# Optimization experiments

Hardware: AMD Instinct MI355X
Metric: run time of the kernel (lower is better)

The kernel has to match this reference:

```python
import jax, jax.numpy as jnp
import numpy as np

N = 6144      # total nodes
G = 32        # graphs
NPG = 192     # nodes per graph (N = G*NPG)
FIN = 32      # num_node_features
FE = 8        # num_edge_features
H = 64        # layers = [64, 64]
HM = 128      # layers_MLP = [128]
C = 2         # num_classes
K = 8         # opts.knn
E = 49152     # given edges
EPS = 1e-5


def _bn(x, g, b):
    # BatchNorm1d in train mode: biased batch stats
    m = x.mean(0)
    v = x.var(0)
    return (x - m) * jax.lax.rsqrt(v + EPS) * g + b


def setup_inputs() -> dict:
    key = jax.random.key(0)
    ks = jax.random.split(key, 24)

    def w(k, shape):
        return (jax.random.normal(k, shape, jnp.float32)
                * (1.0 / np.sqrt(shape[0])).astype(np.float32))

    x = jax.random.normal(ks[0], (N, FIN), jnp.float32)
    edge_index = jax.random.randint(ks[1], (2, E), 0, N)
    edge_attr = jax.random.normal(ks[2], (E, FE), jnp.float32)
    batch = jnp.arange(N, dtype=jnp.int64 if jax.config.jax_enable_x64 else jnp.int32) // NPG
    return dict(
        x=x, edge_index=edge_index, edge_attr=edge_attr, batch=batch,
        # EdgeFeatsConv layer 1: mlp(Linear(2*FIN+FE,H), ReLU, Linear(H,H)) + root weight
        ef_w1=w(ks[3], (2 * FIN + FE, H)), ef_b1=jnp.zeros((H,), jnp.float32),
        ef_w2=w(ks[4], (H, H)), ef_b2=jnp.zeros((H,), jnp.float32),
        ef_wroot=w(ks[5], (FIN, H)),
        bn1_g=jnp.ones((H,), jnp.float32), bn1_b=jnp.zeros((H,), jnp.float32),
        # EdgeConv layer 2: mlp(Linear(2*H,H), ReLU, Linear(H,H)), aggr=max
        ec_w1=w(ks[6], (2 * H, H)), ec_b1=jnp.zeros((H,), jnp.float32),
        ec_w2=w(ks[7], (H, H)), ec_b2=jnp.zeros((H,), jnp.float32),
        bn2_g=jnp.ones((H,), jnp.float32), bn2_b=jnp.zeros((H,), jnp.float32),
        # model2: Linear(H,HM), BN, ReLU, Linear(HM,C)
        m2_w1=w(ks[8], (H, HM)), m2_b1=jnp.zeros((HM,), jnp.float32),
        m2_bng=jnp.ones((HM,), jnp.float32), m2_bnb=jnp.zeros((HM,), jnp.float32),
        m2_w2=w(ks[9], (HM, C)), m2_b2=jnp.zeros((C,), jnp.float32),
    )


def reference(x, edge_index, edge_attr, batch,
              ef_w1, ef_b1, ef_w2, ef_b2, ef_wroot, bn1_g, bn1_b,
              ec_w1, ec_b1, ec_w2, ec_b2, bn2_g, bn2_b,
              m2_w1, m2_b1, m2_bng, m2_bnb, m2_w2, m2_b2):
    src, dst = edge_index[0], edge_index[1]

    # ---- layer 1: EdgeFeatsConv (edge-conditioned message MLP + root weight, aggr=sum)
    m = jnp.concatenate([x[dst], x[src], edge_attr], axis=1) @ ef_w1 + ef_b1
    m = jax.nn.relu(m) @ ef_w2 + ef_b2
    x1 = jax.ops.segment_sum(m, dst, num_segments=N) + x @ ef_wroot
    x1 = _bn(x1, bn1_g, bn1_b)

    # ---- layer 2: dynamic KNN graph (loop=False) + to_undirected, then EdgeConv (aggr=max)
    sq = jnp.sum(x1 * x1, axis=1)
    d2 = sq[:, None] + sq[None, :] - 2.0 * (x1 @ x1.T)       # [N, N]
    d2 = d2.at[jnp.arange(N), jnp.arange(N)].set(jnp.inf)    # no self loops
    _, nbr = jax.lax.top_k(-d2, K)                           # [N, K] nearest neighbors
    dst0 = jnp.repeat(jnp.arange(N), K)
    src0 = nbr.reshape(-1)
    s = jnp.concatenate([src0, dst0])                        # undirected (dups OK: max aggr)
    d = jnp.concatenate([dst0, src0])

    h = jnp.concatenate([x1[d], x1[s] - x1[d]], axis=1) @ ec_w1 + ec_b1
    h = jax.nn.relu(h) @ ec_w2 + ec_b2
    x2 = jax.ops.segment_max(h, d, num_segments=N)
    x2 = _bn(x2, bn2_g, bn2_b)

    # ---- per-graph all-pairs |g_i - g_z| (row order: for z, for i)
    g = x2.reshape(G, NPG, H)
    diff = jnp.abs(g[:, None, :, :] - g[:, :, None, :]).reshape(-1, H)  # [G*NPG*NPG, H]

    # ---- model2 MLP + log_softmax
    h2 = jax.nn.relu(_bn(diff @ m2_w1 + m2_b1, m2_bng, m2_bnb))
    out = h2 @ m2_w2 + m2_b2
    return jax.nn.log_softmax(out, axis=1)
```

## Files before the change

### kernel.cpp

```cpp
#include <hip/hip_runtime.h>

#define NN 6144
#define GG 32
#define NPGc 192
#define FINc 32
#define FEc 8
#define Hc 64
#define HMc 128
#define Kc 8
#define Ec 49152
#define NKc (NN*Kc)
#define RTOTc (GG*NPGc*NPGc)

typedef float f32x4 __attribute__((ext_vector_type(4)));
typedef short bf16x8 __attribute__((ext_vector_type(8)));
typedef unsigned long long u64;

__device__ __forceinline__ unsigned short f2bf(float f){
  unsigned u = __float_as_uint(f);
  unsigned r = u + 0x7fffu + ((u>>16)&1u);
  return (unsigned short)(r>>16);
}
__device__ __forceinline__ unsigned fenc(float f){
  unsigned u = __float_as_uint(f);
  return (u & 0x80000000u) ? ~u : (u | 0x80000000u);
}
__device__ __forceinline__ float fdec(unsigned e){
  unsigned u = (e & 0x80000000u) ? (e & 0x7fffffffu) : ~e;
  return __uint_as_float(u);
}
__device__ __forceinline__ void bub8(u64* t8, u64 k){
#pragma unroll
  for (int q=0;q<8;q++){ u64 cur=t8[q]; u64 lo=(k<cur)?k:cur; u64 hi=(k<cur)?cur:k; t8[q]=lo; k=hi; }
}

__global__ void k_init(float* dbins, float* stats){
  int idx = blockIdx.x*256 + threadIdx.x;
  if (idx < 64*256) dbins[idx] = 0.f;
  if (idx < 768) stats[idx] = 0.f;
}

__global__ __launch_bounds__(256) void k_root(const float* __restrict__ x, const float* __restrict__ wr, float* __restrict__ x1a){
  __shared__ float Ws[FINc*Hc];
  __shared__ float xr[4][FINc];
  int t = threadIdx.x;
  for (int q=t;q<FINc*Hc;q+=256) Ws[q] = wr[q];
  int rg = t>>6, j = t&63;
  int r = blockIdx.x*4 + rg;
  if (j < FINc) xr[rg][j] = x[r*FINc + j];
  __syncthreads();
  float a0=0.f, a1=0.f;
#pragma unroll
  for (int k=0;k<FINc;k+=2){
    a0 = fmaf(xr[rg][k],   Ws[k*Hc+j],     a0);
    a1 = fmaf(xr[rg][k+1], Ws[(k+1)*Hc+j], a1);
  }
  x1a[r*Hc + j] = a0 + a1;
}

__global__ __launch_bounds__(256) void k_eac(const float* __restrict__ ea, const float* __restrict__ w1, float* __restrict__ EAc){
  __shared__ float Wc[FEc*Hc];
  int t = threadIdx.x;
  for (int q=t; q<FEc*Hc; q+=256) Wc[q] = w1[64*Hc + q];
  __syncthreads();
  int idx = blockIdx.x*256 + t;
  int e = idx >> 4, c4 = (idx & 15)*4;
  float av[8];
#pragma unroll
  for (int q=0;q<8;q++) av[q] = ea[e*FEc + q];
  float4 o = {0.f,0.f,0.f,0.f};
#pragma unroll
  for (int q=0;q<8;q++){
    o.x = fmaf(av[q], Wc[q*Hc + c4+0], o.x);
    o.y = fmaf(av[q], Wc[q*Hc + c4+1], o.y);
    o.z = fmaf(av[q], Wc[q*Hc + c4+2], o.z);
    o.w = fmaf(av[q], Wc[q*Hc + c4+3], o.w);
  }
  *(float4*)(EAc + (size_t)e*Hc + c4) = o;
}

__global__ __launch_bounds__(256) void k_p12(const float* __restrict__ x, const float* __restrict__ w1, const float* __restrict__ b1,
                                             float* __restrict__ P1, float* __restrict__ P2){
  __shared__ float xs[16][32];
  int t = threadIdx.x;
  int j = t & 63, w = t >> 6;
  float wa[32], wb[32];
#pragma unroll
  for (int k=0;k<32;k++){
    wa[k] = w1[k*Hc + j];
    wb[k] = w1[(32+k)*Hc + j];
  }
  float b1j = b1[j];
  int nb = blockIdx.x * 16;
  for (int q=t; q<16*32; q+=256) xs[q>>5][q&31] = x[(size_t)(nb + (q>>5))*FINc + (q&31)];
  __syncthreads();
#pragma unroll
  for (int it=0; it<4; it++){
    int nl = it*4 + w;
    float a = b1j, b = 0.f;
#pragma unroll
    for (int k=0;k<32;k++){
      float xv = xs[nl][k];
      a = fmaf(xv, wa[k], a);
      b = fmaf(xv, wb[k], b);
    }
    int n = nb + nl;
    P1[(size_t)n*Hc + j] = a;
    P2[(size_t)n*Hc + j] = b;
  }
}

__global__ void k_zero_cnt(unsigned* rcnt){
  int idx = blockIdx.x*256 + threadIdx.x;
  if (idx < NN) rcnt[idx] = 0u;
}
__global__ void k_cnt_dst(const int* __restrict__ ei, unsigned* __restrict__ rcnt){
  int e = blockIdx.x*256 + threadIdx.x;
  atomicAdd(&rcnt[ei[Ec + e]], 1u);
}
__global__ __launch_bounds__(256) void k_scan(const unsigned* __restrict__ rcnt, unsigned* __restrict__ rptr, unsigned* __restrict__ rcur){
  __shared__ unsigned ps[256];
  int t = threadIdx.x;
  unsigned loc[24];
  unsigned s = 0;
#pragma unroll
  for (int q=0;q<24;q++){ loc[q] = s; s += rcnt[t*24+q]; }
  ps[t] = s;
  __syncthreads();
  for (int off=1; off<256; off<<=1){
    unsigned v = (t>=off)? ps[t-off] : 0u;
    __syncthreads();
    ps[t] += v;
    __syncthreads();
  }
  unsigned base = (t==0)? 0u : ps[t-1];
#pragma unroll
  for (int q=0;q<24;q++){ unsigned v = base + loc[q]; rptr[t*24+q]=v; rcur[t*24+q]=v; }
  if (t==255) rptr[NN] = ps[255];
}
__global__ void k_fill_dst(const int* __restrict__ ei, unsigned* __restrict__ rcur, unsigned* __restrict__ rlist){
  int e = blockIdx.x*256 + threadIdx.x;
  unsigned pos = atomicAdd(&rcur[ei[Ec + e]], 1u);
  rlist[pos] = (unsigned)e;
}
__global__ void k_rev_cnt(const unsigned* __restrict__ nbr, unsigned* __restrict__ rcnt){
  int e = blockIdx.x*256 + threadIdx.x;
  atomicAdd(&rcnt[nbr[e]], 1u);
}
__global__ void k_rev_fill(const unsigned* __restrict__ nbr, unsigned* __restrict__ rcur, unsigned* __restrict__ rlist){
  int e = blockIdx.x*256 + threadIdx.x;
  unsigned pos = atomicAdd(&rcur[nbr[e]], 1u);
  rlist[pos] = (unsigned)(e >> 3);
}

__global__ __launch_bounds__(128) void k_node1(const float* __restrict__ P1, const float* __restrict__ P2, const float* __restrict__ EAc,
        const int* __restrict__ ei, const unsigned* __restrict__ rptr, const unsigned* __restrict__ rlist,
        const float* __restrict__ w2, const float* __restrict__ b2, float* __restrict__ x1a){
  __shared__ __align__(16) float accs[16][68];
  __shared__ __align__(16) float W2T[64][68];
  __shared__ unsigned rp_s[17];
  int t = threadIdx.x;
  int d0 = blockIdx.x * 16;
  for (int q=t; q<64*64; q+=128) W2T[q&63][q>>6] = w2[q];
  if (t < 17) rp_s[t] = rptr[d0 + t];
  __syncthreads();
  int slot = t>>3, cg = t&7, c0 = cg*8;
  int n = d0 + slot;
  float4 p1a = *(const float4*)(P1 + (size_t)n*Hc + c0);
  float4 p1b = *(const float4*)(P1 + (size_t)n*Hc + c0 + 4);
  float acc[8];
#pragma unroll
  for (int q=0;q<8;q++) acc[q] = 0.f;
  unsigned beg = rp_s[slot], end = rp_s[slot+1];
  for (unsigned pos=beg; pos<end; pos++){
    unsigned e = rlist[pos];
    int s = ei[e];
    float4 qa = *(const float4*)(P2 + (size_t)s*Hc + c0);
    float4 qb = *(const float4*)(P2 + (size_t)s*Hc + c0 + 4);
    float4 fa = *(const float4*)(EAc + (size_t)e*Hc + c0);
    float4 fb = *(const float4*)(EAc + (size_t)e*Hc + c0 + 4);
    acc[0] += fmaxf(p1a.x + qa.x + fa.x, 0.f);
    acc[1] += fmaxf(p1a.y + qa.y + fa.y, 0.f);
    acc[2] += fmaxf(p1a.z + qa.z + fa.z, 0.f);
    acc[3] += fmaxf(p1a.w + qa.w + fa.w, 0.f);
    acc[4] += fmaxf(p1b.x + qb.x + fb.x, 0.f);
    acc[5] += fmaxf(p1b.y + qb.y + fb.y, 0.f);
    acc[6] += fmaxf(p1b.z + qb.z + fb.z, 0.f);
    acc[7] += fmaxf(p1b.w + qb.w + fb.w, 0.f);
  }
  *(float4*)&accs[slot][c0]   = make_float4(acc[0],acc[1],acc[2],acc[3]);
  *(float4*)&accs[slot][c0+4] = make_float4(acc[4],acc[5],acc[6],acc[7]);
  __syncthreads();
  float out[8];
#pragma unroll
  for (int q=0;q<8;q++) out[q] = 0.f;
  for (int k4=0;k4<16;k4++){
    float4 hv = *(const float4*)&accs[slot][k4*4];
#pragma unroll
    for (int cc=0;cc<8;cc++){
      float4 wv = *(const float4*)&W2T[c0+cc][k4*4];
      out[cc] = fmaf(hv.x,wv.x, fmaf(hv.y,wv.y, fmaf(hv.z,wv.z, fmaf(hv.w,wv.w, out[cc]))));
    }
  }
  float deg = (float)(end - beg);
  float* px = x1a + (size_t)n*Hc + c0;
#pragma unroll
  for (int cc=0;cc<8;cc++) px[cc] += out[cc] + deg*b2[c0+cc];
}

__global__ __launch_bounds__(256) void k_bn_stats(const float* __restrict__ src, float* __restrict__ gsum, float* __restrict__ gss){
  int t = threadIdx.x;
  int c = t & 63;
  int r0 = blockIdx.x*64 + (t>>6);
  float s=0.f, ss=0.f;
  for (int it=0; it<16; it++){
    int r = r0 + it*4;
    float v = src[r*Hc + c];
    s += v; ss += v*v;
  }
  __shared__ float S[64], SS[64];
  if (t < 64){ S[t]=0.f; SS[t]=0.f; }
  __syncthreads();
  atomicAdd(&S[c], s); atomicAdd(&SS[c], ss);
  __syncthreads();
  if (t < 64){ atomicAdd(&gsum[t], S[t]); atomicAdd(&gss[t], SS[t]); }
}

__global__ void k_bn_fin(const float* gsum, const float* gss, const float* gam, const float* bet, float* sc, float* sh){
  int c = threadIdx.x;
  float mean = gsum[c] / (float)NN;
  float var  = gss[c] / (float)NN - mean*mean;
  float rs = rsqrtf(var + 1e-5f);
  float s = rs * gam[c];
  sc[c] = s; sh[c] = bet[c] - mean*s;
}

__global__ __launch_bounds__(256) void k_apply_bn1_sq(const float* __restrict__ x1a, const float* __restrict__ sc, const float* __restrict__ sh,
                               float* __restrict__ x1bn, float* __restrict__ sqv){
  int t = threadIdx.x;
  int c = t & 63;
  int r = blockIdx.x*4 + (t>>6);
  float v = x1a[r*Hc + c]*sc[c] + sh[c];
  x1bn[r*Hc + c] = v;
  float s = v*v;
#pragma unroll
  for (int off=1; off<64; off<<=1) s += __shfl_xor(s, off, 64);
  if (c == 0) sqv[r] = s;
}

__global__ __launch_bounds__(128,2) void k_knn(const float* __restrict__ x1bn, const float* __restrict__ sqv, u64* __restrict__ parts, int CH){
  __shared__ __align__(16) float XJ[64][68];
  __shared__ float sqj[64];
  int t = threadIdx.x;
  int i1 = blockIdx.x*256 + t;
  int i2 = i1 + 128;
  float4 xa[16], xb[16];
#pragma unroll
  for (int q=0;q<16;q++){
    xa[q] = *(const float4*)(x1bn + (size_t)i1*Hc + q*4);
    xb[q] = *(const float4*)(x1bn + (size_t)i2*Hc + q*4);
  }
  float sqi1 = sqv[i1], sqi2 = sqv[i2];
  u64 t8a[8], t8b[8];
#pragma unroll
  for (int q=0;q<8;q++){ t8a[q] = ~0ull; t8b[q] = ~0ull; }
  float thra = __uint_as_float(0x7f800000u);
  float thrb = thra;
  int cpc = NN / CH;
  int nsub = cpc >> 6;
  int jbase0 = blockIdx.y * cpc;
  for (int sub=0; sub<nsub; sub++){
    int jb = jbase0 + sub*64;
    __syncthreads();
    {
      int c = t>>1, hh = t&1;
      const float4* srcp = (const float4*)(x1bn + (size_t)(jb + c)*Hc + hh*32);
#pragma unroll
      for (int q=0;q<8;q++) *(float4*)&XJ[c][hh*32 + q*4] = srcp[q];
      if (t < 64) sqj[t] = sqv[jb + t];
    }
    __syncthreads();
    for (int j=0;j<64;j++){
      float sqjc = sqj[j];
      float a0=0.f,a1=0.f,a2=0.f,a3=0.f,b0=0.f,b1=0.f,b2=0.f,b3=0.f;
#pragma unroll
      for (int q4=0;q4<4;q4++){
        float4 xj0 = *(const float4*)&XJ[j][q4*16];
        float4 xj1 = *(const float4*)&XJ[j][q4*16+4];
        float4 xj2 = *(const float4*)&XJ[j][q4*16+8];
        float4 xj3 = *(const float4*)&XJ[j][q4*16+12];
        float4 A0 = xa[q4*4+0], A1 = xa[q4*4+1], A2v = xa[q4*4+2], A3 = xa[q4*4+3];
        float4 B0 = xb[q4*4+0], B1 = xb[q4*4+1], B2v = xb[q4*4+2], B3 = xb[q4*4+3];
        a0=fmaf(A0.x,xj0.x,a0); a1=fmaf(A0.y,xj0.y,a1); a2=fmaf(A0.z,xj0.z,a2); a3=fmaf(A0.w,xj0.w,a3);
        b0=fmaf(B0.x,xj0.x,b0); b1=fmaf(B0.y,xj0.y,b1); b2=fmaf(B0.z,xj0.z,b2); b3=fmaf(B0.w,xj0.w,b3);
        a0=fmaf(A1.x,xj1.x,a0); a1=fmaf(A1.y,xj1.y,a1); a2=fmaf(A1.z,xj1.z,a2); a3=fmaf(A1.w,xj1.w,a3);
        b0=fmaf(B1.x,xj1.x,b0); b1=fmaf(B1.y,xj1.y,b1); b2=fmaf(B1.z,xj1.z,b2); b3=fmaf(B1.w,xj1.w,b3);
        a0=fmaf(A2v.x,xj2.x,a0); a1=fmaf(A2v.y,xj2.y,a1); a2=fmaf(A2v.z,xj2.z,a2); a3=fmaf(A2v.w,xj2.w,a3);
        b0=fmaf(B2v.x,xj2.x,b0); b1=fmaf(B2v.y,xj2.y,b1); b2=fmaf(B2v.z,xj2.z,b2); b3=fmaf(B2v.w,xj2.w,b3);
        a0=fmaf(A3.x,xj3.x,a0); a1=fmaf(A3.y,xj3.y,a1); a2=fmaf(A3.z,xj3.z,a2); a3=fmaf(A3.w,xj3.w,a3);
        b0=fmaf(B3.x,xj3.x,b0); b1=fmaf(B3.y,xj3.y,b1); b2=fmaf(B3.z,xj3.z,b2); b3=fmaf(B3.w,xj3.w,b3);
      }
      float dot1 = (a0+a1)+(a2+a3);
      float dot2 = (b0+b1)+(b2+b3);
      int jj = jb + j;
      float d2a = (sqi1 + sqjc) - 2.f*dot1;
      float d2b = (sqi2 + sqjc) - 2.f*dot2;
      bool ia = !(d2a > thra) && (jj != i1);
      bool ib = !(d2b > thrb) && (jj != i2);
      if (__builtin_expect(ia | ib, 0)){
        if (ia){
          u64 ka = (((u64)fenc(d2a))<<32) | (unsigned)jj;
          bub8(t8a, ka);
          thra = fdec((unsigned)(t8a[7]>>32));
        }
        if (ib){
          u64 kb = (((u64)fenc(d2b))<<32) | (unsigned)jj;
          bub8(t8b, kb);
          thrb = fdec((unsigned)(t8b[7]>>32));
        }
      }
    }
  }
  u64* pa = parts + ((size_t)blockIdx.y*NN + i1)*8;
  u64* pb = parts + ((size_t)blockIdx.y*NN + i2)*8;
#pragma unroll
  for (int q=0;q<8;q++){ pa[q] = t8a[q]; pb[q] = t8b[q]; }
}

__global__ __launch_bounds__(256) void k_knn_merge(const u64* __restrict__ parts, int CH, unsigned* __restrict__ nbr){
  int r = blockIdx.x*256 + threadIdx.x;
  u64 t8[8];
#pragma unroll
  for (int q=0;q<8;q++) t8[q] = ~0ull;
  for (int ch=0; ch<CH; ch++){
    const u64* p = parts + ((size_t)ch*NN + r)*8;
    u64 k[8];
#pragma unroll
    for (int q=0;q<8;q++) k[q] = p[q];
#pragma unroll
    for (int q=0;q<8;q++){
      if (k[q] >= t8[7]) break;
      bub8(t8, k[q]);
    }
  }
#pragma unroll
  for (int s=0;s<8;s++) nbr[r*Kc + s] = (unsigned)(t8[s] & 0xffffffffu);
}

__global__ __launch_bounds__(256) void k_pq(const float* __restrict__ x1bn, const float* __restrict__ w1, const float* __restrict__ b1,
                                            float* __restrict__ A2, float* __restrict__ Qm){
  __shared__ float xs[16][64];
  int t = threadIdx.x;
  int j = t & 63, w = t >> 6;
  float wa[64], wb[64];
#pragma unroll
  for (int k=0;k<64;k++){
    float wt  = w1[k*64 + j];
    float wbv = w1[(64+k)*64 + j];
    wa[k] = wt - wbv; wb[k] = wbv;
  }
  float b1j = b1[j];
  int nb = blockIdx.x * 16;
  for (int q=t; q<16*64; q+=256) xs[q>>6][q&63] = x1bn[(size_t)(nb + (q>>6))*64 + (q&63)];
  __syncthreads();
#pragma unroll
  for (int it=0; it<4; it++){
    int nl = it*4 + w;
    float a = b1j, qq = 0.f;
#pragma unroll
    for (int k=0;k<64;k++){
      float xv = xs[nl][k];
      a  = fmaf(xv, wa[k], a);
      qq = fmaf(xv, wb[k], qq);
    }
    int n = nb + nl;
    A2[(size_t)n*64 + j] = a;
    Qm[(size_t)n*64 + j] = qq;
  }
}

__global__ __launch_bounds__(128) void k_edge2max(const float* __restrict__ A2, const float* __restrict__ Qm,
        const unsigned* __restrict__ nbr, const unsigned* __restrict__ rptr, const unsigned* __restrict__ rlist,
        const float* __restrict__ w2, const float* __restrict__ b2, float* __restrict__ x2f){
  __shared__ __align__(16) float W2T[64][68];
  __shared__ __align__(16) float hidT[64][132];
  __shared__ unsigned x2s[17][64];
  __shared__ unsigned rp_s[17];
  __shared__ int wslot[128];
  int t = threadIdx.x;
  int d0 = blockIdx.x * 16;
  for (int q=t; q<64*64; q+=128) W2T[q&63][q>>6] = w2[q];
  for (int q=t; q<17*64; q+=128) ((unsigned*)x2s)[q] = 0x007FFFFFu;
  if (t < 17) rp_s[t] = rptr[d0 + t];
  __syncthreads();
  unsigned rp0 = rp_s[0];
  int total_rev = (int)(rp_s[16] - rp0);
  int eg = t & 15, cg = t >> 4;
  int r0 = eg*8, c0 = cg*8;
  float b2v[8];
#pragma unroll
  for (int cc=0;cc<8;cc++) b2v[cc] = b2[c0+cc];
  int ntile = 1 + ((total_rev + 127) >> 7);
  for (int tile=0; tile<ntile; tile++){
    int d, s, active;
    if (tile == 0){
      d = d0 + (t>>3); s = (int)nbr[(size_t)d*8 + (t&7)]; active = 1; wslot[t] = t>>3;
    } else {
      int idx = (tile-1)*128 + t;
      active = idx < total_rev;
      if (active){
        unsigned pos = rp0 + (unsigned)idx;
        int sl = 0;
#pragma unroll
        for (int m=1; m<16; m++) sl += (pos >= rp_s[m]) ? 1 : 0;
        s = (int)rlist[pos];
        d = d0 + sl;
        wslot[t] = sl;
      } else { d = d0; s = 0; wslot[t] = 16; }
    }
    if (active){
      const float* pa = A2 + (size_t)d*64;
      const float* pq = Qm + (size_t)s*64;
#pragma unroll
      for (int c4=0; c4<16; c4++){
        float4 va = *(const float4*)(pa + c4*4);
        float4 vq = *(const float4*)(pq + c4*4);
        hidT[c4*4+0][t] = fmaxf(va.x+vq.x, 0.f);
        hidT[c4*4+1][t] = fmaxf(va.y+vq.y, 0.f);
        hidT[c4*4+2][t] = fmaxf(va.z+vq.z, 0.f);
        hidT[c4*4+3][t] = fmaxf(va.w+vq.w, 0.f);
      }
    } else {
#pragma unroll
      for (int c4=0; c4<16; c4++){
        hidT[c4*4+0][t] = 0.f; hidT[c4*4+1][t] = 0.f;
        hidT[c4*4+2][t] = 0.f; hidT[c4*4+3][t] = 0.f;
      }
    }
    __syncthreads();
    float acc[8][8];
#pragma unroll
    for (int i=0;i<8;i++)
#pragma unroll
      for (int cc=0;cc<8;cc++) acc[i][cc] = 0.f;
    for (int k=0;k<64;k+=4){
      float4 wv[8];
#pragma unroll
      for (int cc=0;cc<8;cc++) wv[cc] = *(const float4*)&W2T[c0+cc][k];
#pragma unroll
      for (int kk=0;kk<4;kk++){
        float4 h0 = *(const float4*)&hidT[k+kk][r0];
        float4 h1 = *(const float4*)&hidT[k+kk][r0+4];
        float hh[8] = {h0.x,h0.y,h0.z,h0.w,h1.x,h1.y,h1.z,h1.w};
#pragma unroll
        for (int i=0;i<8;i++)
#pragma unroll
          for (int cc=0;cc<8;cc++)
            acc[i][cc] = fmaf(hh[i], ((const float*)&wv[cc])[kk], acc[i][cc]);
      }
    }
    int cur = wslot[r0];
    float mx[8];
#pragma unroll
    for (int cc=0;cc<8;cc++) mx[cc] = acc[0][cc];
    for (int i=1;i<8;i++){
      int sl = wslot[r0+i];
      if (sl != cur){
#pragma unroll
        for (int cc=0;cc<8;cc++) atomicMax(&x2s[cur][c0+cc], fenc(mx[cc] + b2v[cc]));
        cur = sl;
#pragma unroll
        for (int cc=0;cc<8;cc++) mx[cc] = acc[i][cc];
      } else {
#pragma unroll
        for (int cc=0;cc<8;cc++) mx[cc] = fmaxf(mx[cc], acc[i][cc]);
      }
    }
#pragma unroll
    for (int cc=0;cc<8;cc++) atomicMax(&x2s[cur][c0+cc], fenc(mx[cc] + b2v[cc]));
    __syncthreads();
  }
#pragma unroll
  for (int q=0;q<8;q++){
    int idx = t + q*128;
    int sl = idx >> 6, c = idx & 63;
    x2f[(size_t)(d0+sl)*64 + c] = fdec(x2s[sl][c]);
  }
}

__global__ __launch_bounds__(256) void k_apply_bn2f(const float* __restrict__ x2f, const float* __restrict__ sc, const float* __restrict__ sh, float* __restrict__ x2bn){
  int idx = blockIdx.x*256 + threadIdx.x;
  int c = idx & 63;
  x2bn[idx] = x2f[idx]*sc[c] + sh[c];
}

__global__ __launch_bounds__(256,2) void k_d_stats(const float* __restrict__ x2bn, const float* __restrict__ w1, float* __restrict__ dbins){
  __shared__ __align__(16) char sm[24576 + 16384 + 1024];
  unsigned char* A = (unsigned char*)sm;
  unsigned char* W = (unsigned char*)sm + 24576;
  float* Ssum = (float*)(sm + 40960);
  int t = threadIdx.x;
  int gid = blockIdx.x; int g = gid / NPGc; int z = gid - g*NPGc;
  const float* xg = x2bn + (size_t)g*NPGc*Hc;
  const float* xz = xg + z*Hc;
  Ssum[t] = 0.f;
#pragma unroll
  for (int q=0;q<8;q++){
    int task = t + 256*q; int c = task & 127; int c4 = task >> 7;
    ushort4 p;
    p.x = f2bf(w1[(4*c4+0)*HMc + c]);
    p.y = f2bf(w1[(4*c4+1)*HMc + c]);
    p.z = f2bf(w1[(4*c4+2)*HMc + c]);
    p.w = f2bf(w1[(4*c4+3)*HMc + c]);
    *(ushort4*)(W + c*128 + ((c4*8) ^ ((c&7)<<4))) = p;
  }
#pragma unroll
  for (int q=0;q<12;q++){
    int task = t + 256*q; int i = task >> 4; int c = task & 15;
    float4 a = *(const float4*)(xg + i*Hc + c*4);
    float4 b = *(const float4*)(xz + c*4);
    ushort4 p;
    p.x = f2bf(fabsf(a.x-b.x)); p.y = f2bf(fabsf(a.y-b.y));
    p.z = f2bf(fabsf(a.z-b.z)); p.w = f2bf(fabsf(a.w-b.w));
    *(ushort4*)(A + i*128 + ((c*8) ^ ((i&7)<<4))) = p;
  }
  __syncthreads();
  int w = t>>6, l = t&63, lr = l&15, lg = l>>4;
  int sw = (lr&7)<<4;
  f32x4 zero = {0.f,0.f,0.f,0.f};
  f32x4 acc[3][8];
#pragma unroll
  for (int r=0;r<3;r++)
#pragma unroll
    for (int c=0;c<8;c++) acc[r][c] = zero;
#pragma unroll
  for (int kk=0;kk<2;kk++){
    bf16x8 af[3], bfr[8];
#pragma unroll
    for (int r=0;r<3;r++){
      int row = (w*3+r)*16 + lr;
      af[r] = *(const bf16x8*)(A + row*128 + ((lg*16 + 64*kk) ^ sw));
    }
#pragma unroll
    for (int c=0;c<8;c++){
      int col = c*16 + lr;
      bfr[c] = *(const bf16x8*)(W + col*128 + ((lg*16 + 64*kk) ^ sw));
    }
#pragma unroll
    for (int r=0;r<3;r++)
#pragma unroll
      for (int c=0;c<8;c++)
        acc[r][c] = __builtin_amdgcn_mfma_f32_16x16x32_bf16(af[r], bfr[c], acc[r][c], 0,0,0);
  }
#pragma unroll
  for (int c=0;c<8;c++){
    int col = c*16 + lr;
    float s=0.f, ss=0.f;
#pragma unroll
    for (int r=0;r<3;r++)
#pragma unroll
      for (int q=0;q<4;q++){ float v = acc[r][c][q]; s += v; ss = fmaf(v,v,ss); }
    s  += __shfl_xor(s, 16, 64);  ss += __shfl_xor(ss, 16, 64);
    s  += __shfl_xor(s, 32, 64);  ss += __shfl_xor(ss, 32, 64);
    if (lg == 0){
      atomicAdd(&Ssum[col], s);
      atomicAdd(&Ssum[128+col], ss);
    }
  }
  __syncthreads();
  if (t < 128){
    int bin = gid & 63;
    atomicAdd(&dbins[bin*256 + t], Ssum[t]);
    atomicAdd(&dbins[bin*256 + 128 + t], Ssum[128+t]);
  }
}

__global__ void k_d_fin(const float* __restrict__ dbins, const float* gam, const float* bet, float* dsc, float* dsh){
  int c = threadIdx.x;
  float s=0.f, ss=0.f;
#pragma unroll 8
  for (int b=0;b<64;b++){ s += dbins[b*256 + c]; ss += dbins[b*256 + 128 + c]; }
  float mean = s / (float)RTOTc;
  float var  = ss / (float)RTOTc - mean*mean;
  float rs = rsqrtf(var + 1e-5f);
  float k = rs * gam[c];
  dsc[c] = k; dsh[c] = bet[c] - mean*k;
}

__global__ __launch_bounds__(256,2) void k_d_main(const float* __restrict__ x2bn, const float* __restrict__ w1,
                         const float* __restrict__ w2, const float* __restrict__ b2g,
                         const float* __restrict__ dsc, const float* __restrict__ dsh, float* __restrict__ out){
  __shared__ __align__(16) char sm[49152 + 4096 + 1024];
  unsigned char* A   = (unsigned char*)sm;
  unsigned char* W   = (unsigned char*)sm + 24576;
  unsigned char* W2T = (unsigned char*)sm + 49152;
  float* sS = (float*)(sm + 53248);
  int t = threadIdx.x;
  int gid = blockIdx.x; int g = gid / NPGc; int z = gid - g*NPGc;
  const float* xg = x2bn + (size_t)g*NPGc*Hc;
  const float* xz = xg + z*Hc;
  if (t < 128){ sS[t] = dsc[t]; sS[128+t] = dsh[t]; }
  {
    int c = t>>4, kc = t&15;
    ushort4 p0 = make_ushort4(0,0,0,0), p1 = make_ushort4(0,0,0,0);
    if (c < 2){
      p0.x = f2bf(w2[(kc*8+0)*2 + c]); p0.y = f2bf(w2[(kc*8+1)*2 + c]);
      p0.z = f2bf(w2[(kc*8+2)*2 + c]); p0.w = f2bf(w2[(kc*8+3)*2 + c]);
      p1.x = f2bf(w2[(kc*8+4)*2 + c]); p1.y = f2bf(w2[(kc*8+5)*2 + c]);
      p1.z = f2bf(w2[(kc*8+6)*2 + c]); p1.w = f2bf(w2[(kc*8+7)*2 + c]);
    }
    int byte = c*256 + ((kc*16) ^ ((c&7)<<4));
    *(ushort4*)(W2T + byte) = p0;
    *(ushort4*)(W2T + byte + 8) = p1;
  }
#pragma unroll
  for (int q=0;q<8;q++){
    int task = t + 256*q; int c = task & 127; int c4 = task >> 7;
    ushort4 p;
    p.x = f2bf(w1[(4*c4+0)*HMc + c]);
    p.y = f2bf(w1[(4*c4+1)*HMc + c]);
    p.z = f2bf(w1[(4*c4+2)*HMc + c]);
    p.w = f2bf(w1[(4*c4+3)*HMc + c]);
    *(ushort4*)(W + c*128 + ((c4*8) ^ ((c&7)<<4))) = p;
  }
#pragma unroll
  for (int q=0;q<12;q++){
    int task = t + 256*q; int i = task >> 4; int c = task & 15;
    float4 a = *(const float4*)(xg + i*Hc + c*4);
    float4 b = *(const float4*)(xz + c*4);
    ushort4 p;
    p.x = f2bf(fabsf(a.x-b.x)); p.y = f2bf(fabsf(a.y-b.y));
    p.z = f2bf(fabsf(a.z-b.z)); p.w = f2bf(fabsf(a.w-b.w));
    *(ushort4*)(A + i*128 + ((c*8) ^ ((i&7)<<4))) = p;
  }
  __syncthreads();
  int w = t>>6, l = t&63, lr = l&15, lg = l>>4;
  int sw = (lr&7)<<4;
  f32x4 zero = {0.f,0.f,0.f,0.f};
  f32x4 acc[3][8];
#pragma unroll
  for (int r=0;r<3;r++)
#pragma unroll
    for (int c=0;c<8;c++) acc[r][c] = zero;
#pragma unroll
  for (int kk=0;kk<2;kk++){
    bf16x8 af[3], bfr[8];
#pragma unroll
    for (int r=0;r<3;r++){
      int row = (w*3+r)*16 + lr;
      af[r] = *(const bf16x8*)(A + row*128 + ((lg*16 + 64*kk) ^ sw));
    }
#pragma unroll
    for (int c=0;c<8;c++){
      int col = c*16 + lr;
      bfr[c] = *(const bf16x8*)(W + col*128 + ((lg*16 + 64*kk) ^ sw));
    }
#pragma unroll
    for (int r=0;r<3;r++)
#pragma unroll
      for (int c=0;c<8;c++)
        acc[r][c] = __builtin_amdgcn_mfma_f32_16x16x32_bf16(af[r], bfr[c], acc[r][c], 0,0,0);
  }
  __syncthreads();
#pragma unroll
  for (int r=0;r<3;r++){
#pragma unroll
    for (int c=0;c<8;c++){
      int col = c*16 + lr;
      float scl = sS[col], shf = sS[128+col];
#pragma unroll
      for (int q=0;q<4;q++){
        int row = (w*3+r)*16 + lg*4 + q;
        float v = fmaxf(acc[r][c][q]*scl + shf, 0.f);
        *(unsigned short*)(A + row*256 + ((col*2) ^ ((row&7)<<4))) = f2bf(v);
      }
    }
  }
  __syncthreads();
  f32x4 acc2[3];
#pragma unroll
  for (int r=0;r<3;r++) acc2[r] = zero;
#pragma unroll
  for (int kk=0;kk<4;kk++){
    bf16x8 bw = *(const bf16x8*)(W2T + lr*256 + ((lg*16 + 64*kk) ^ sw));
#pragma unroll
    for (int r=0;r<3;r++){
      int row = (w*3+r)*16 + lr;
      bf16x8 ah = *(const bf16x8*)(A + row*256 + ((lg*16 + 64*kk) ^ sw));
      acc2[r] = __builtin_amdgcn_mfma_f32_16x16x32_bf16(ah, bw, acc2[r], 0,0,0);
    }
  }
  float b2a = b2g[0], b2b = b2g[1];
  size_t obase = (size_t)gid * NPGc;
#pragma unroll
  for (int r=0;r<3;r++){
#pragma unroll
    for (int q=0;q<4;q++){
      float o = acc2[r][q];
      float oo = __shfl_xor(o, 1, 64);
      if (lr < 2){
        int row = (w*3+r)*16 + lg*4 + q;
        float self = o + ((lr==0) ? b2a : b2b);
        float oth  = oo + ((lr==0) ? b2b : b2a);
        float mx = fmaxf(self, oth);
        float lse = mx + logf(expf(self-mx) + expf(oth-mx));
        out[(obase + row)*2 + lr] = self - lse;
      }
    }
  }
}

extern "C" void kernel_launch(void* const* d_in, const int* in_sizes, int n_in,
                              void* d_out, int out_size, void* d_ws, size_t ws_size,
                              hipStream_t stream){
  const float* x    = (const float*)d_in[0];
  const int*   ei   = (const int*)d_in[1];
  const float* ea   = (const float*)d_in[2];
  const float* efw1 = (const float*)d_in[4];
  const float* efb1 = (const float*)d_in[5];
  const float* efw2 = (const float*)d_in[6];
  const float* efb2 = (const float*)d_in[7];
  const float* efwr = (const float*)d_in[8];
  const float* bn1g = (const float*)d_in[9];
  const float* bn1b = (const float*)d_in[10];
  const float* ecw1 = (const float*)d_in[11];
  const float* ecb1 = (const float*)d_in[12];
  const float* ecw2 = (const float*)d_in[13];
  const float* ecb2 = (const float*)d_in[14];
  const float* bn2g = (const float*)d_in[15];
  const float* bn2b = (const float*)d_in[16];
  const float* m2w1 = (const float*)d_in[17];
  const float* m2bng = (const float*)d_in[19];
  const float* m2bnb = (const float*)d_in[20];
  const float* m2w2  = (const float*)d_in[21];
  const float* m2b2  = (const float*)d_in[22];

  char* ws = (char*)d_ws;
  float*    x1a   = (float*)(ws + 0);
  float*    x1bn  = (float*)(ws + 1572864);
  float*    x2bn  = (float*)(ws + 3145728);
  float*    x2f   = (float*)(ws + 4718592);
  float*    sqv   = (float*)(ws + 6291456);
  unsigned* nbr   = (unsigned*)(ws + 6316032);
  float*    stats = (float*)(ws + 6512640);
  float*    dbins = (float*)(ws + 6515712);
  u64*      parts = (u64*)(ws + 6581248);
  float*    A2    = (float*)(ws + 0);
  float*    Qm    = (float*)(ws + 3145728);
  float*    P1    = (float*)(ws + 3145728);
  float*    P2    = (float*)(ws + 4718592);
  unsigned* rcnt  = (unsigned*)(ws + 6581248);
  unsigned* rptr  = rcnt + 6400;
  unsigned* rcur  = rptr + 6400;
  unsigned* rlist = rcur + 6400;
  float*    EAc   = (float*)(ws + 6581248 + 4194304);
  float *g1sum = stats,     *g1ss = stats+64,  *sc1 = stats+128, *sh1 = stats+192;
  float *g2sum = stats+256, *g2ss = stats+320, *sc2 = stats+384, *sh2 = stats+448;
  float *dsc = stats+512, *dsh = stats+640;
  float* outp = (float*)d_out;

  int CH = 96;
  if (ws_size < 6581248ull + (size_t)NN*96*64) CH = 48;
  if (ws_size < 6581248ull + (size_t)NN*48*64) CH = 24;

  k_init<<<64,256,0,stream>>>(dbins, stats);
  k_root<<<1536,256,0,stream>>>(x, efwr, x1a);
  k_eac<<<3072,256,0,stream>>>(ea, efw1, EAc);
  k_zero_cnt<<<24,256,0,stream>>>(rcnt);
  k_cnt_dst<<<192,256,0,stream>>>(ei, rcnt);
  k_scan<<<1,256,0,stream>>>(rcnt, rptr, rcur);
  k_fill_dst<<<192,256,0,stream>>>(ei, rcur, rlist);
  k_p12<<<384,256,0,stream>>>(x, efw1, efb1, P1, P2);
  k_node1<<<384,128,0,stream>>>(P1, P2, EAc, ei, rptr, rlist, efw2, efb2, x1a);
  k_bn_stats<<<96,256,0,stream>>>(x1a, g1sum, g1ss);
  k_bn_fin<<<1,64,0,stream>>>(g1sum, g1ss, bn1g, bn1b, sc1, sh1);
  k_apply_bn1_sq<<<1536,256,0,stream>>>(x1a, sc1, sh1, x1bn, sqv);
  dim3 kg(24, CH);
  k_knn<<<kg,128,0,stream>>>(x1bn, sqv, parts, CH);
  k_knn_merge<<<24,256,0,stream>>>(parts, CH, nbr);
  k_zero_cnt<<<24,256,0,stream>>>(rcnt);
  k_rev_cnt<<<192,256,0,stream>>>(nbr, rcnt);
  k_scan<<<1,256,0,stream>>>(rcnt, rptr, rcur);
  k_rev_fill<<<192,256,0,stream>>>(nbr, rcur, rlist);
  k_pq<<<384,256,0,stream>>>(x1bn, ecw1, ecb1, A2, Qm);
  k_edge2max<<<384,128,0,stream>>>(A2, Qm, nbr, rptr, rlist, ecw2, ecb2, x2f);
  k_bn_stats<<<96,256,0,stream>>>(x2f, g2sum, g2ss);
  k_bn_fin<<<1,64,0,stream>>>(g2sum, g2ss, bn2g, bn2b, sc2, sh2);
  k_apply_bn2f<<<1536,256,0,stream>>>(x2f, sc2, sh2, x2bn);
  k_d_stats<<<6144,256,0,stream>>>(x2bn, m2w1, dbins);
  k_d_fin<<<1,128,0,stream>>>(dbins, m2bng, m2bnb, dsc, dsh);
  k_d_main<<<6144,256,0,stream>>>(x2bn, m2w1, m2w2, m2b2, dsc, dsh, outp);
}
```

Before: 554.1 us.

## Precompute bf16 MLP weights, fuse BN finalize, split KNN merge into two stages

Adds a one-time kernel that converts and swizzles the model2 weights to bf16, so the 6144-block d_stats and d_main kernels just copy them into shared memory instead of converting per block. BN finalize kernels are removed and their math is folded into the apply kernels. The KNN partial merge is split into a parallel group merge plus a final 8-way merge, and the number of KNN column chunks is reduced to 48. This trades extra workspace and per-block redundant BN math for fewer launches and more merge parallelism.

```diff
diff --git a/kernel.cpp b/kernel.cpp
--- a/kernel.cpp
+++ b/kernel.cpp
@@ -38,6 +38,33 @@
   int idx = blockIdx.x*256 + threadIdx.x;
   if (idx < 64*256) dbins[idx] = 0.f;
   if (idx < 768) stats[idx] = 0.f;
+}
+
+__global__ void k_prep_w(const float* __restrict__ w1, const float* __restrict__ w2,
+                         unsigned short* __restrict__ Wpre, unsigned short* __restrict__ W2Tp){
+  int idx = blockIdx.x*256 + threadIdx.x;
+  if (idx < 2048){
+    int c = idx >> 4, c4 = idx & 15;
+    ushort4 p;
+    p.x = f2bf(w1[(4*c4+0)*HMc + c]);
+    p.y = f2bf(w1[(4*c4+1)*HMc + c]);
+    p.z = f2bf(w1[(4*c4+2)*HMc + c]);
+    p.w = f2bf(w1[(4*c4+3)*HMc + c]);
+    *(ushort4*)((char*)Wpre + c*128 + ((c4*8) ^ ((c&7)<<4))) = p;
+  } else if (idx < 2304){
+    int t2 = idx - 2048;
+    int c = t2>>4, kc = t2&15;
+    ushort4 p0 = make_ushort4(0,0,0,0), p1 = make_ushort4(0,0,0,0);
+    if (c < 2){
+      p0.x = f2bf(w2[(kc*8+0)*2 + c]); p0.y = f2bf(w2[(kc*8+1)*2 + c]);
+      p0.z = f2bf(w2[(kc*8+2)*2 + c]); p0.w = f2bf(w2[(kc*8+3)*2 + c]);
+      p1.x = f2bf(w2[(kc*8+4)*2 + c]); p1.y = f2bf(w2[(kc*8+5)*2 + c]);
+      p1.z = f2bf(w2[(kc*8+6)*2 + c]); p1.w = f2bf(w2[(kc*8+7)*2 + c]);
+    }
+    int byte = c*256 + ((kc*16) ^ ((c&7)<<4));
+    *(ushort4*)((char*)W2Tp + byte) = p0;
+    *(ushort4*)((char*)W2Tp + byte + 8) = p1;
+  }
 }
 
 __global__ __launch_bounds__(256) void k_root(const float* __restrict__ x, const float* __restrict__ wr, float* __restrict__ x1a){
@@ -226,21 +253,23 @@
   if (t < 64){ atomicAdd(&gsum[t], S[t]); atomicAdd(&gss[t], SS[t]); }
 }
 
-__global__ void k_bn_fin(const float* gsum, const float* gss, const float* gam, const float* bet, float* sc, float* sh){
-  int c = threadIdx.x;
-  float mean = gsum[c] / (float)NN;
-  float var  = gss[c] / (float)NN - mean*mean;
-  float rs = rsqrtf(var + 1e-5f);
-  float s = rs * gam[c];
-  sc[c] = s; sh[c] = bet[c] - mean*s;
-}
-
-__global__ __launch_bounds__(256) void k_apply_bn1_sq(const float* __restrict__ x1a, const float* __restrict__ sc, const float* __restrict__ sh,
+__global__ __launch_bounds__(256) void k_apply_bn1_sq(const float* __restrict__ x1a,
+                               const float* __restrict__ gsum, const float* __restrict__ gss,
+                               const float* __restrict__ gam, const float* __restrict__ bet,
                                float* __restrict__ x1bn, float* __restrict__ sqv){
-  int t = threadIdx.x;
+  __shared__ float scs[64], shs[64];
+  int t = threadIdx.x;
+  if (t < 64){
+    float mean = gsum[t] / (float)NN;
+    float var  = gss[t] / (float)NN - mean*mean;
+    float rs = rsqrtf(var + 1e-5f);
+    float s = rs * gam[t];
+    scs[t] = s; shs[t] = bet[t] - mean*s;
+  }
+  __syncthreads();
   int c = t & 63;
   int r = blockIdx.x*4 + (t>>6);
-  float v = x1a[r*Hc + c]*sc[c] + sh[c];
+  float v = x1a[r*Hc + c]*scs[c] + shs[c];
   x1bn[r*Hc + c] = v;
   float s = v*v;
 #pragma unroll
@@ -327,13 +356,35 @@
   for (int q=0;q<8;q++){ pa[q] = t8a[q]; pb[q] = t8b[q]; }
 }
 
-__global__ __launch_bounds__(256) void k_knn_merge(const u64* __restrict__ parts, int CH, unsigned* __restrict__ nbr){
+__global__ __launch_bounds__(256) void k_knn_merge1(const u64* __restrict__ parts, int CPG, u64* __restrict__ parts2){
+  int g = blockIdx.x / 24;
+  int r = (blockIdx.x % 24)*256 + threadIdx.x;
+  u64 t8[8];
+#pragma unroll
+  for (int q=0;q<8;q++) t8[q] = ~0ull;
+  for (int ch=g*CPG; ch<(g+1)*CPG; ch++){
+    const u64* p = parts + ((size_t)ch*NN + r)*8;
+    u64 k[8];
+#pragma unroll
+    for (int q=0;q<8;q++) k[q] = p[q];
+#pragma unroll
+    for (int q=0;q<8;q++){
+      if (k[q] >= t8[7]) break;
+      bub8(t8, k[q]);
+    }
+  }
+  u64* o = parts2 + ((size_t)g*NN + r)*8;
+#pragma unroll
+  for (int q=0;q<8;q++) o[q] = t8[q];
+}
+
+__global__ __launch_bounds__(256) void k_knn_merge2(const u64* __restrict__ parts2, unsigned* __restrict__ nbr){
   int r = blockIdx.x*256 + threadIdx.x;
   u64 t8[8];
 #pragma unroll
   for (int q=0;q<8;q++) t8[q] = ~0ull;
-  for (int ch=0; ch<CH; ch++){
-    const u64* p = parts + ((size_t)ch*NN + r)*8;
+  for (int g=0; g<8; g++){
+    const u64* p = parts2 + ((size_t)g*NN + r)*8;
     u64 k[8];
 #pragma unroll
     for (int q=0;q<8;q++) k[q] = p[q];
@@ -488,13 +539,26 @@
   }
 }
 
-__global__ __launch_bounds__(256) void k_apply_bn2f(const float* __restrict__ x2f, const float* __restrict__ sc, const float* __restrict__ sh, float* __restrict__ x2bn){
-  int idx = blockIdx.x*256 + threadIdx.x;
+__global__ __launch_bounds__(256) void k_apply_bn2f(const float* __restrict__ x2f,
+                               const float* __restrict__ gsum, const float* __restrict__ gss,
+                               const float* __restrict__ gam, const float* __restrict__ bet,
+                               float* __restrict__ x2bn){
+  __shared__ float scs[64], shs[64];
+  int t = threadIdx.x;
+  if (t < 64){
+    float mean = gsum[t] / (float)NN;
+    float var  = gss[t] / (float)NN - mean*mean;
+    float rs = rsqrtf(var + 1e-5f);
+    float s = rs * gam[t];
+    scs[t] = s; shs[t] = bet[t] - mean*s;
+  }
+  __syncthreads();
+  int idx = blockIdx.x*256 + t;
   int c = idx & 63;
-  x2bn[idx] = x2f[idx]*sc[c] + sh[c];
-}
-
-__global__ __launch_bounds__(256,2) void k_d_stats(const float* __restrict__ x2bn, const float* __restrict__ w1, float* __restrict__ dbins){
+  x2bn[idx] = x2f[idx]*scs[c] + shs[c];
+}
+
+__global__ __launch_bounds__(256,2) void k_d_stats(const float* __restrict__ x2bn, const unsigned short* __restrict__ Wpre, float* __restrict__ dbins){
   __shared__ __align__(16) char sm[24576 + 16384 + 1024];
   unsigned char* A = (unsigned char*)sm;
   unsigned char* W = (unsigned char*)sm + 24576;
@@ -505,15 +569,8 @@
   const float* xz = xg + z*Hc;
   Ssum[t] = 0.f;
 #pragma unroll
-  for (int q=0;q<8;q++){
-    int task = t + 256*q; int c = task & 127; int c4 = task >> 7;
-    ushort4 p;
-    p.x = f2bf(w1[(4*c4+0)*HMc + c]);
-    p.y = f2bf(w1[(4*c4+1)*HMc + c]);
-    p.z = f2bf(w1[(4*c4+2)*HMc + c]);
-    p.w = f2bf(w1[(4*c4+3)*HMc + c]);
-    *(ushort4*)(W + c*128 + ((c4*8) ^ ((c&7)<<4))) = p;
-  }
+  for (int q=0;q<4;q++)
+    *(float4*)(W + t*16 + q*4096) = *(const float4*)((const char*)Wpre + t*16 + q*4096);
 #pragma unroll
   for (int q=0;q<12;q++){
     int task = t + 256*q; int i = task >> 4; int c = task & 15;
@@ -587,8 +644,8 @@
   dsc[c] = k; dsh[c] = bet[c] - mean*k;
 }
 
-__global__ __launch_bounds__(256,2) void k_d_main(const float* __restrict__ x2bn, const float* __restrict__ w1,
-                         const float* __restrict__ w2, const float* __restrict__ b2g,
+__global__ __launch_bounds__(256,2) void k_d_main(const float* __restrict__ x2bn, const unsigned short* __restrict__ Wpre,
+                         const unsigned short* __restrict__ W2Tp, const float* __restrict__ b2g,
                          const float* __restrict__ dsc, const float* __restrict__ dsh, float* __restrict__ out){
   __shared__ __align__(16) char sm[49152 + 4096 + 1024];
   unsigned char* A   = (unsigned char*)sm;
@@ -600,29 +657,10 @@
   const float* xg = x2bn + (size_t)g*NPGc*Hc;
   const float* xz = xg + z*Hc;
   if (t < 128){ sS[t] = dsc[t]; sS[128+t] = dsh[t]; }
-  {
-    int c = t>>4, kc = t&15;
-    ushort4 p0 = make_ushort4(0,0,0,0), p1 = make_ushort4(0,0,0,0);
-    if (c < 2){
-      p0.x = f2bf(w2[(kc*8+0)*2 + c]); p0.y = f2bf(w2[(kc*8+1)*2 + c]);
-      p0.z = f2bf(w2[(kc*8+2)*2 + c]); p0.w = f2bf(w2[(kc*8+3)*2 + c]);
-      p1.x = f2bf(w2[(kc*8+4)*2 + c]); p1.y = f2bf(w2[(kc*8+5)*2 + c]);
-      p1.z = f2bf(w2[(kc*8+6)*2 + c]); p1.w = f2bf(w2[(kc*8+7)*2 + c]);
-    }
-    int byte = c*256 + ((kc*16) ^ ((c&7)<<4));
-    *(ushort4*)(W2T + byte) = p0;
-    *(ushort4*)(W2T + byte + 8) = p1;
-  }
-#pragma unroll
-  for (int q=0;q<8;q++){
-    int task = t + 256*q; int c = task & 127; int c4 = task >> 7;
-    ushort4 p;
-    p.x = f2bf(w1[(4*c4+0)*HMc + c]);
-    p.y = f2bf(w1[(4*c4+1)*HMc + c]);
-    p.z = f2bf(w1[(4*c4+2)*HMc + c]);
-    p.w = f2bf(w1[(4*c4+3)*HMc + c]);
-    *(ushort4*)(W + c*128 + ((c4*8) ^ ((c&7)<<4))) = p;
-  }
+  *(float4*)(W2T + t*16) = *(const float4*)((const char*)W2Tp + t*16);
+#pragma unroll
+  for (int q=0;q<4;q++)
+    *(float4*)(W + t*16 + q*4096) = *(const float4*)((const char*)Wpre + t*16 + q*4096);
 #pragma unroll
   for (int q=0;q<12;q++){
     int task = t + 256*q; int i = task >> 4; int c = task & 15;
@@ -754,16 +792,23 @@
   unsigned* rcur  = rptr + 6400;
   unsigned* rlist = rcur + 6400;
   float*    EAc   = (float*)(ws + 6581248 + 4194304);
-  float *g1sum = stats,     *g1ss = stats+64,  *sc1 = stats+128, *sh1 = stats+192;
-  float *g2sum = stats+256, *g2ss = stats+320, *sc2 = stats+384, *sh2 = stats+448;
+  float *g1sum = stats,     *g1ss = stats+64;
+  float *g2sum = stats+256, *g2ss = stats+320;
   float *dsc = stats+512, *dsh = stats+640;
   float* outp = (float*)d_out;
 
-  int CH = 96;
-  if (ws_size < 6581248ull + (size_t)NN*96*64) CH = 48;
-  if (ws_size < 6581248ull + (size_t)NN*48*64) CH = 24;
+  int CH = 48;
+  if (ws_size < 6581248ull + (size_t)NN*48*64 + 3145728ull + 20480ull) CH = 24;
+  if (ws_size < 6581248ull + (size_t)NN*24*64 + 3145728ull + 20480ull) CH = 16;
+  size_t parts2_off = 6581248ull + (size_t)CH*NN*64;
+  size_t wpre_off = parts2_off + 3145728ull;
+  if (wpre_off < 23358464ull) wpre_off = 23358464ull;
+  u64* parts2 = (u64*)(ws + parts2_off);
+  unsigned short* Wpre  = (unsigned short*)(ws + wpre_off);
+  unsigned short* W2Tp  = (unsigned short*)(ws + wpre_off + 16384);
 
   k_init<<<64,256,0,stream>>>(dbins, stats);
+  k_prep_w<<<9,256,0,stream>>>(m2w1, m2w2, Wpre, W2Tp);
   k_root<<<1536,256,0,stream>>>(x, efwr, x1a);
   k_eac<<<3072,256,0,stream>>>(ea, efw1, EAc);
   k_zero_cnt<<<24,256,0,stream>>>(rcnt);
@@ -773,11 +818,11 @@
   k_p12<<<384,256,0,stream>>>(x, efw1, efb1, P1, P2);
   k_node1<<<384,128,0,stream>>>(P1, P2, EAc, ei, rptr, rlist, efw2, efb2, x1a);
   k_bn_stats<<<96,256,0,stream>>>(x1a, g1sum, g1ss);
-  k_bn_fin<<<1,64,0,stream>>>(g1sum, g1ss, bn1g, bn1b, sc1, sh1);
-  k_apply_bn1_sq<<<1536,256,0,stream>>>(x1a, sc1, sh1, x1bn, sqv);
+  k_apply_bn1_sq<<<1536,256,0,stream>>>(x1a, g1sum, g1ss, bn1g, bn1b, x1bn, sqv);
   dim3 kg(24, CH);
   k_knn<<<kg,128,0,stream>>>(x1bn, sqv, parts, CH);
-  k_knn_merge<<<24,256,0,stream>>>(parts, CH, nbr);
+  k_knn_merge1<<<192,256,0,stream>>>(parts, CH/8, parts2);
+  k_knn_merge2<<<24,256,0,stream>>>(parts2, nbr);
   k_zero_cnt<<<24,256,0,stream>>>(rcnt);
   k_rev_cnt<<<192,256,0,stream>>>(nbr, rcnt);
   k_scan<<<1,256,0,stream>>>(rcnt, rptr, rcur);
@@ -785,9 +830,8 @@
   k_pq<<<384,256,0,stream>>>(x1bn, ecw1, ecb1, A2, Qm);
   k_edge2max<<<384,128,0,stream>>>(A2, Qm, nbr, rptr, rlist, ecw2, ecb2, x2f);
   k_bn_stats<<<96,256,0,stream>>>(x2f, g2sum, g2ss);
-  k_bn_fin<<<1,64,0,stream>>>(g2sum, g2ss, bn2g, bn2b, sc2, sh2);
-  k_apply_bn2f<<<1536,256,0,stream>>>(x2f, sc2, sh2, x2bn);
-  k_d_stats<<<6144,256,0,stream>>>(x2bn, m2w1, dbins);
+  k_apply_bn2f<<<1536,256,0,stream>>>(x2f, g2sum, g2ss, bn2g, bn2b, x2bn);
+  k_d_stats<<<6144,256,0,stream>>>(x2bn, Wpre, dbins);
   k_d_fin<<<1,128,0,stream>>>(dbins, m2bng, m2bnb, dsc, dsh);
-  k_d_main<<<6144,256,0,stream>>>(x2bn, m2w1, m2w2, m2b2, dsc, dsh, outp);
-}
+  k_d_main<<<6144,256,0,stream>>>(x2bn, Wpre, W2Tp, m2b2, dsc, dsh, outp);
+}
```

Measured after the change: 511.5 us. 1.08x faster.
